# Optimization experiments

Measured on AMD Instinct MI355X. Metric: run time of the kernel, lower is better.

## Reference

```python
import jax, jax.numpy as jnp
import numpy as np

N = 6144
IN_F = 256
OUT_F = 64
ALPHA = 0.2  # leaky relu slope
NEG_INF = -9e15
ADJ_DENSITY = 0.01


def setup_inputs() -> dict:
    key = jax.random.key(0)
    kx, ka, kw, kat, ks, ke = jax.random.split(key, 6)
    x = jax.random.normal(kx, (N, IN_F), dtype=jnp.float32)
    adj = (jax.random.uniform(ka, (N, N)) < ADJ_DENSITY).astype(jnp.float32)
    adj = adj.at[jnp.arange(N), jnp.arange(N)].set(0.0)
    # xavier-uniform-ish init scale (gain 1.414)
    def xavier(k, shape):
        fan_in, fan_out = shape[0], shape[1]
        lim = 1.414 * np.sqrt(6.0 / (fan_in + fan_out))
        return jax.random.uniform(k, shape, minval=-lim, maxval=lim, dtype=jnp.float32)
    W = xavier(kw, (IN_F, OUT_F))
    a = xavier(kat, (2 * OUT_F, 1))
    W_si = xavier(ks, (1, 1))
    W_ei = xavier(ke, (1, 1))
    return {"x": x, "adj": adj, "W": W, "a": a, "W_si": W_si, "W_ei": W_ei}


def reference(x, adj, W, a, W_si, W_ei):
    # h: [N, F_out]
    h = x @ W
    # additive GAT score: e[i,j] = leakyrelu(Wh1[i] + Wh2[j])
    Wh1 = h @ a[:OUT_F, :]           # [N, 1]
    Wh2 = h @ a[OUT_F:, :]           # [N, 1]
    e = jax.nn.leaky_relu(Wh1 + Wh2.T, negative_slope=ALPHA)  # [N, N]
    # adjacency-power topology bias
    adj2 = adj @ adj
    adj3 = adj2 @ adj
    adj_w = adj + adj2 + adj3
    adj_w = adj_w.at[jnp.arange(N), jnp.arange(N)].set(0.0)
    e = jnp.abs(W_ei) * e + jnp.abs(W_si) * adj_w
    # masked softmax over neighbors (row-wise)
    scores = jnp.where(adj > 0, e, NEG_INF)
    attention = jax.nn.softmax(scores, axis=1)
    # dropout omitted (eval mode / training=False)
    h_prime = attention @ h
    return jax.nn.elu(h_prime)
```

## Files before the change

kernel.cpp:

```cpp
#include <hip/hip_runtime.h>
#include <math.h>

#define N 6144
#define MAXD 128
#define NWORDS 96
#define NW32 192

typedef unsigned long long u64;
typedef unsigned int u32;
typedef unsigned char u8;
typedef float f4 __attribute__((ext_vector_type(4)));


__device__ __forceinline__ int a_addr(int j) {
    int vdx = (j & ~255) | ((j & 3) << 6) | ((j >> 2) & 63);
    return (((vdx >> 2) & 7) << 10) | ((vdx >> 5) << 2) | (vdx & 3);
}

#define FA(s, c, a, b, ci) { u32 _t = (a) ^ (b); (s) = _t ^ (ci); (c) = ((a) & (b)) | ((ci) & _t); }

template <int START>
__device__ __forceinline__ void badd_from(u32* p, u32 cy) {
    #pragma unroll
    for (int q = START; q < 6; ++q) { u32 x = p[q] & cy; p[q] ^= cy; cy = x; }
    p[6] ^= cy;
}

__device__ __forceinline__ void csa15(u32* p, const u32* x) {
    u32 s0,c0,s1,c1,s2,c2,s3,c3,s4,c4;
    FA(s0,c0, x[0], x[1], x[2]);
    FA(s1,c1, x[3], x[4], x[5]);
    FA(s2,c2, x[6], x[7], x[8]);
    FA(s3,c3, x[9], x[10], x[11]);
    FA(s4,c4, x[12], x[13], x[14]);
    u32 t0,d0,u0,d1;
    FA(t0,d0, s0, s1, s2);
    FA(u0,d1, s3, s4, t0);
    u32 e0,f0,e1,f1,e2,f2;
    FA(e0,f0, c0, c1, c2);
    FA(e1,f1, c3, c4, d0);
    FA(e2,f2, e0, e1, d1);
    u32 g0,h0;
    FA(g0,h0, f0, f1, f2);
    badd_from<0>(p, u0);
    badd_from<1>(p, e2);
    badd_from<2>(p, g0);
    badd_from<3>(p, h0);
}

__device__ __forceinline__ u64 bit_transpose64(u64 x, int lane) {
    const u64 masks[6] = {0xAAAAAAAAAAAAAAAAull, 0xCCCCCCCCCCCCCCCCull,
                          0xF0F0F0F0F0F0F0F0ull, 0xFF00FF00FF00FF00ull,
                          0xFFFF0000FFFF0000ull, 0xFFFFFFFF00000000ull};
    #pragma unroll
    for (int k = 0; k < 6; ++k) {
        int s = 1 << k;
        u64 m = masks[k];
        u64 y = (u64)__shfl_xor((long long)x, s, 64);
        x = (lane & s) ? ((x & m) | ((y & m) >> s))
                       : ((x & ~m) | ((y & ~m) << s));
    }
    return x;
}

__global__ __launch_bounds__(256) void k_build(
    const float* __restrict__ adj,
    u64* __restrict__ rowbits, int* __restrict__ row_cnt, int* __restrict__ row_list)
{
    int i = blockIdx.x;
    int t = threadIdx.x, w = t >> 6, lane = t & 63;
    __shared__ int wtot[4];

    const f4* ar = (const f4*)(adj + (long)i * N) + (w * 6) * 64;

    f4 v[6];
    #pragma unroll
    for (int c = 0; c < 6; ++c)
        v[c] = __builtin_nontemporal_load(ar + c * 64 + lane);

    u64 m[6][4];
    #pragma unroll
    for (int c = 0; c < 6; ++c) {
        m[c][0] = __ballot(v[c].x != 0.0f);
        m[c][1] = __ballot(v[c].y != 0.0f);
        m[c][2] = __ballot(v[c].z != 0.0f);
        m[c][3] = __ballot(v[c].w != 0.0f);
    }

    int tot = 0;
    #pragma unroll
    for (int c = 0; c < 6; ++c) {
        #pragma unroll
        for (int p = 0; p < 4; ++p) tot += __popcll(m[c][p]);
    }
    if (lane == 0) wtot[w] = tot;
    __syncthreads();
    int base = 0;
    #pragma unroll
    for (int q = 0; q < 4; ++q) if (q < w) base += wtot[q];

    u64* rb = rowbits + (long)i * NWORDS + w * 24;
    #pragma unroll
    for (int c = 0; c < 6; ++c) {
        #pragma unroll
        for (int p = 0; p < 4; ++p) {
            u64 mm = m[c][p];
            if (lane == 0) rb[c * 4 + p] = mm;
            if ((mm >> lane) & 1ull) {
                int rank = __popcll(mm & ((1ull << lane) - 1ull));
                int s = base + rank;
                int j = (w * 6 + c) * 256 + (lane << 2) + p;
                if (s < MAXD) row_list[(long)i * MAXD + s] = j;
            }
            base += __popcll(mm);
        }
    }
    if (t == 0) {
        int tt = wtot[0] + wtot[1] + wtot[2] + wtot[3];
        row_cnt[i] = tt < 127 ? tt : 127;
    }
}

__global__ __launch_bounds__(256) void k_trans_gemm(
    const u64* __restrict__ rowbits, u64* __restrict__ colbits,
    const float* __restrict__ x, const float* __restrict__ W,
    const float* __restrict__ a,
    float* __restrict__ h, float* __restrict__ Wh1, float* __restrict__ Wh2)
{
    __shared__ float Wl[128 * 64];
    __shared__ float xt[8][256];

    int t = threadIdx.x, w = t >> 6, lane = t & 63;
    int bid = blockIdx.x;

    if (bid < 2304) {
        int tile = bid * 4 + w;
        int tr = tile / 96, tc = tile - tr * 96;
        u64 v = rowbits[(long)(tr * 64 + lane) * NWORDS + tc];
        v = bit_transpose64(v, lane);
        colbits[(long)(tc * 64 + lane) * NWORDS + tr] = v;
        return;
    }

    long i0 = (long)(bid - 2304) * 8;

    {
        const float4* xs = (const float4*)(x + i0 * 256);
        float4* xd = (float4*)&xt[0][0];
        xd[t]       = xs[t];
        xd[256 + t] = xs[256 + t];
    }

    float acc0 = 0.f, acc1 = 0.f;
    int r0 = w * 2;

    #pragma unroll
    for (int half = 0; half < 2; ++half) {
        __syncthreads();
        {
            const float4* Ws = (const float4*)(W + half * 128 * 64);
            float4* Wd = (float4*)Wl;
            #pragma unroll
            for (int q = 0; q < 8; ++q) Wd[q * 256 + t] = Ws[q * 256 + t];
        }
        __syncthreads();
        const float* xr0 = &xt[r0][half * 128];
        const float* xr1 = &xt[r0 + 1][half * 128];
        #pragma unroll 8
        for (int kk = 0; kk < 128; ++kk) {
            float wv = Wl[kk * 64 + lane];
            acc0 = fmaf(xr0[kk], wv, acc0);
            acc1 = fmaf(xr1[kk], wv, acc1);
        }
    }

    h[(i0 + r0)     * 64 + lane] = acc0;
    h[(i0 + r0 + 1) * 64 + lane] = acc1;
    float a1 = a[lane], a2 = a[64 + lane];
    float s10 = acc0 * a1, s20 = acc0 * a2;
    float s11 = acc1 * a1, s21 = acc1 * a2;
    #pragma unroll
    for (int off = 32; off; off >>= 1) {
        s10 += __shfl_xor(s10, off, 64);
        s20 += __shfl_xor(s20, off, 64);
        s11 += __shfl_xor(s11, off, 64);
        s21 += __shfl_xor(s21, off, 64);
    }
    if (lane == 0) {
        Wh1[i0 + r0]     = s10;  Wh2[i0 + r0]     = s20;
        Wh1[i0 + r0 + 1] = s11;  Wh2[i0 + r0 + 1] = s21;
    }
}

__global__ __launch_bounds__(256) void k_collist(
    const u64* __restrict__ colbits,
    int* __restrict__ col_cnt, int* __restrict__ col_list)
{
    int w = threadIdx.x >> 6, lane = threadIdx.x & 63;
    int v = blockIdx.x * 4 + w;
    int j = (v & ~255) | ((v & 63) << 2) | ((v >> 6) & 3);

    u64 w0 = 0, w1 = 0;
    if (lane < 48) {
        const u64* p2 = colbits + (long)v * NWORDS + lane * 2;
        w0 = p2[0]; w1 = p2[1];
    }
    int pc = __popcll(w0) + __popcll(w1);
    int incl = pc;
    #pragma unroll
    for (int off = 1; off < 64; off <<= 1) {
        int y = __shfl_up(incl, off, 64);
        if (lane >= off) incl += y;
    }
    int excl = incl - pc;
    int total = __shfl(incl, 63, 64);
    if (lane == 0) col_cnt[j] = total;

    int* cl = col_list + (long)j * MAXD;
    int s = excl;
    int ibase = lane * 128;
    while (w0) {
        int b = __ffsll((long long)w0) - 1; w0 &= w0 - 1;
        if (s < MAXD) cl[s] = a_addr(ibase + b);
        ++s;
    }
    ibase += 64;
    while (w1) {
        int b = __ffsll((long long)w1) - 1; w1 &= w1 - 1;
        if (s < MAXD) cl[s] = a_addr(ibase + b);
        ++s;
    }
}

__global__ __launch_bounds__(256) void k_attn(
    const float* __restrict__ h, const float* __restrict__ Wh1, const float* __restrict__ Wh2,
    const u64* __restrict__ rowbits,
    const int* __restrict__ row_cnt, const int* __restrict__ row_list,
    const int* __restrict__ col_cnt, const int* __restrict__ col_list,
    const float* __restrict__ W_si, const float* __restrict__ W_ei,
    float* __restrict__ out)
{
    __shared__ u32 adj2p[8 * 256];
    __shared__ int nbr[MAXD];
    __shared__ int ccbuf[MAXD];
    __shared__ float lrbuf[MAXD];
    __shared__ float ebuf[MAXD];
    __shared__ float part[256];
    __shared__ float sh_max, sh_sum;

    int i = blockIdx.x;
    int t = threadIdx.x, w = t >> 6, lane = t & 63;
    int deg = row_cnt[i];
    deg = deg < 127 ? deg : 127;

    if (deg == 0) {
        float acc = 0.f;
        for (int r = w; r < N; r += 4) acc += h[(long)r * 64 + lane];
        part[t] = acc;
        __syncthreads();
        if (w == 0) {
            float s = part[lane] + part[64 + lane] + part[128 + lane] + part[192 + lane];
            s *= (1.0f / N);
            out[(long)i * 64 + lane] = s > 0.f ? s : expm1f(s);
        }
        return;
    }

    float aWei = fabsf(W_ei[0]);
    float aWsi = fabsf(W_si[0]);

    if (t < deg) {
        int j = row_list[(long)i * MAXD + t];
        nbr[t] = j;
        int cc = col_cnt[j];
        ccbuf[t] = cc < MAXD ? cc : MAXD;
        float z = Wh1[i] + Wh2[j];
        lrbuf[t] = aWei * (z > 0.f ? z : 0.2f * z);
    }

    if (t < NW32) {
        const u32* rb32 = (const u32*)rowbits;
        const int* rl = row_list + (long)i * MAXD;
        u32 p[7] = {0,0,0,0,0,0,0};

        int m = 0;
        for (; m + 15 <= deg; m += 15) {
            u32 x[15];
            #pragma unroll
            for (int q = 0; q < 15; ++q) {
                int j = rl[m + q];
                x[q] = rb32[(long)j * NW32 + t];
            }
            csa15(p, x);
        }
        if (m < deg) {
            u32 x[15];
            #pragma unroll
            for (int q = 0; q < 15; ++q) {
                int mq = m + q;
                int j = rl[mq < deg ? mq : 0];
                u32 vv = rb32[(long)j * NW32 + t];
                x[q] = (mq < deg) ? vv : 0u;
            }
            csa15(p, x);
        }

        #pragma unroll
        for (int g = 0; g < 8; ++g) {
            u32 acc = 0;
            #pragma unroll
            for (int pl = 0; pl < 7; ++pl) {
                u32 nib = (p[pl] >> (4 * g)) & 0xFu;
                acc += (nib * (0x00204081u << pl)) & (0x01010101u << pl);
            }
            adj2p[g * 256 + t] = acc;
        }
    }
    __syncthreads();

    const u8* adj2b = (const u8*)adj2p;

    {
        int g = t >> 3, sub = t & 7;
        for (int e = g; e < deg; e += 32) {
            int cc = ccbuf[e];
            const int* cl = col_list + (long)nbr[e] * MAXD;
            u32 a30 = 0, a31 = 0, a32 = 0, a33 = 0;
            int q = sub;
            for (; q + 24 < cc; q += 32) {
                int k0 = cl[q];
                int k1 = cl[q + 8];
                int k2 = cl[q + 16];
                int k3 = cl[q + 24];
                a30 += (u32)adj2b[k0];
                a31 += (u32)adj2b[k1];
                a32 += (u32)adj2b[k2];
                a33 += (u32)adj2b[k3];
            }
            if (q + 8 < cc) {
                int k0 = cl[q];
                int k1 = cl[q + 8];
                a30 += (u32)adj2b[k0];
                a31 += (u32)adj2b[k1];
                q += 16;
            }
            if (q < cc) a32 += (u32)adj2b[cl[q]];
            u32 a3 = (a30 + a31) + (a32 + a33);
            a3 += __shfl_xor(a3, 1, 64);
            a3 += __shfl_xor(a3, 2, 64);
            a3 += __shfl_xor(a3, 4, 64);
            if (sub == 0) {
                u32 a2 = (u32)adj2b[a_addr(nbr[e])];
                ebuf[e] = lrbuf[e] + aWsi * (float)(1u + a2 + a3);
            }
        }
    }
    __syncthreads();

    if (w == 0) {
        float v = -3.4e38f;
        for (int idx = lane; idx < deg; idx += 64) v = fmaxf(v, ebuf[idx]);
        #pragma unroll
        for (int off = 32; off; off >>= 1) v = fmaxf(v, __shfl_xor(v, off, 64));
        if (lane == 0) sh_max = v;
    }
    __syncthreads();
    if (t < deg) ebuf[t] = expf(ebuf[t] - sh_max);
    __syncthreads();
    if (w == 0) {
        float s = 0.f;
        for (int idx = lane; idx < deg; idx += 64) s += ebuf[idx];
        #pragma unroll
        for (int off = 32; off; off >>= 1) s += __shfl_xor(s, off, 64);
        if (lane == 0) sh_sum = s;
    }
    __syncthreads();

    float acc0 = 0.f, acc1 = 0.f;
    int e = w;
    for (; e + 4 < deg; e += 8) {
        acc0 = fmaf(ebuf[e],     h[(long)nbr[e]     * 64 + lane], acc0);
        acc1 = fmaf(ebuf[e + 4], h[(long)nbr[e + 4] * 64 + lane], acc1);
    }
    if (e < deg)
        acc0 = fmaf(ebuf[e], h[(long)nbr[e] * 64 + lane], acc0);
    part[t] = acc0 + acc1;
    __syncthreads();
    if (w == 0) {
        float s = part[lane] + part[64 + lane] + part[128 + lane] + part[192 + lane];
        s /= sh_sum;
        out[(long)i * 64 + lane] = s > 0.f ? s : expm1f(s);
    }
}

extern "C" void kernel_launch(void* const* d_in, const int* in_sizes, int n_in,
                              void* d_out, int out_size, void* d_ws, size_t ws_size,
                              hipStream_t stream) {
    const float* x    = (const float*)d_in[0];
    const float* adj  = (const float*)d_in[1];
    const float* W    = (const float*)d_in[2];
    const float* a    = (const float*)d_in[3];
    const float* W_si = (const float*)d_in[4];
    const float* W_ei = (const float*)d_in[5];
    float* out = (float*)d_out;

    char* ws = (char*)d_ws;
    size_t off = 0;
    auto alloc = [&](size_t bytes) -> void* {
        void* p = ws + off;
        off += (bytes + 255) & ~(size_t)255;
        return p;
    };
    u64*   rowbits  = (u64*)  alloc((size_t)N * NWORDS * sizeof(u64));
    u64*   colbits  = (u64*)  alloc((size_t)N * NWORDS * sizeof(u64));
    float* h        = (float*)alloc((size_t)N * 64 * sizeof(float));
    float* Wh1      = (float*)alloc((size_t)N * sizeof(float));
    float* Wh2      = (float*)alloc((size_t)N * sizeof(float));
    int*   row_cnt  = (int*)  alloc((size_t)N * sizeof(int));
    int*   row_list = (int*)  alloc((size_t)N * MAXD * sizeof(int));
    int*   col_cnt  = (int*)  alloc((size_t)N * sizeof(int));
    int*   col_list = (int*)  alloc((size_t)N * MAXD * sizeof(int));

    k_build     <<<N, 256, 0, stream>>>(adj, rowbits, row_cnt, row_list);
    k_trans_gemm<<<2304 + 768, 256, 0, stream>>>(rowbits, colbits, x, W, a, h, Wh1, Wh2);
    k_collist   <<<N / 4, 256, 0, stream>>>(colbits, col_cnt, col_list);
    k_attn      <<<N, 256, 0, stream>>>(h, Wh1, Wh2, rowbits, row_cnt, row_list,
                                        col_cnt, col_list, W_si, W_ei, out);
}
```

Measured before the change: 294.0 us.

## Compute adj2 row via shared-memory atomic scatter instead of bitsliced CSA popcount

Replaces the bit-sliced carry-save adder that summed neighbor row bitmaps (reading 768 bytes per neighbor) with a sparse scatter. Each neighbor's row list is walked and a 6144-entry shared-memory counter is incremented with atomics. Column lists now store plain indices and the adj3 pass reads 32-bit counters. This trades dense bitmap loads and ALU work for about deg^2 LDS atomics and a 24KB shared buffer that must be zeroed per block, which may reduce occupancy.

```diff
diff --git a/kernel.cpp b/kernel.cpp
--- a/kernel.cpp
+++ b/kernel.cpp
@@ -4,49 +4,12 @@
 #define N 6144
 #define MAXD 128
 #define NWORDS 96
-#define NW32 192
 
 typedef unsigned long long u64;
 typedef unsigned int u32;
 typedef unsigned char u8;
 typedef float f4 __attribute__((ext_vector_type(4)));
 
-
-__device__ __forceinline__ int a_addr(int j) {
-    int vdx = (j & ~255) | ((j & 3) << 6) | ((j >> 2) & 63);
-    return (((vdx >> 2) & 7) << 10) | ((vdx >> 5) << 2) | (vdx & 3);
-}
-
-#define FA(s, c, a, b, ci) { u32 _t = (a) ^ (b); (s) = _t ^ (ci); (c) = ((a) & (b)) | ((ci) & _t); }
-
-template <int START>
-__device__ __forceinline__ void badd_from(u32* p, u32 cy) {
-    #pragma unroll
-    for (int q = START; q < 6; ++q) { u32 x = p[q] & cy; p[q] ^= cy; cy = x; }
-    p[6] ^= cy;
-}
-
-__device__ __forceinline__ void csa15(u32* p, const u32* x) {
-    u32 s0,c0,s1,c1,s2,c2,s3,c3,s4,c4;
-    FA(s0,c0, x[0], x[1], x[2]);
-    FA(s1,c1, x[3], x[4], x[5]);
-    FA(s2,c2, x[6], x[7], x[8]);
-    FA(s3,c3, x[9], x[10], x[11]);
-    FA(s4,c4, x[12], x[13], x[14]);
-    u32 t0,d0,u0,d1;
-    FA(t0,d0, s0, s1, s2);
-    FA(u0,d1, s3, s4, t0);
-    u32 e0,f0,e1,f1,e2,f2;
-    FA(e0,f0, c0, c1, c2);
-    FA(e1,f1, c3, c4, d0);
-    FA(e2,f2, e0, e1, d1);
-    u32 g0,h0;
-    FA(g0,h0, f0, f1, f2);
-    badd_from<0>(p, u0);
-    badd_from<1>(p, e2);
-    badd_from<2>(p, g0);
-    badd_from<3>(p, h0);
-}
 
 __device__ __forceinline__ u64 bit_transpose64(u64 x, int lane) {
     const u64 masks[6] = {0xAAAAAAAAAAAAAAAAull, 0xCCCCCCCCCCCCCCCCull,
@@ -221,28 +184,28 @@
     int ibase = lane * 128;
     while (w0) {
         int b = __ffsll((long long)w0) - 1; w0 &= w0 - 1;
-        if (s < MAXD) cl[s] = a_addr(ibase + b);
+        if (s < MAXD) cl[s] = ibase + b;
         ++s;
     }
     ibase += 64;
     while (w1) {
         int b = __ffsll((long long)w1) - 1; w1 &= w1 - 1;
-        if (s < MAXD) cl[s] = a_addr(ibase + b);
+        if (s < MAXD) cl[s] = ibase + b;
         ++s;
     }
 }
 
 __global__ __launch_bounds__(256) void k_attn(
     const float* __restrict__ h, const float* __restrict__ Wh1, const float* __restrict__ Wh2,
-    const u64* __restrict__ rowbits,
     const int* __restrict__ row_cnt, const int* __restrict__ row_list,
     const int* __restrict__ col_cnt, const int* __restrict__ col_list,
     const float* __restrict__ W_si, const float* __restrict__ W_ei,
     float* __restrict__ out)
 {
-    __shared__ u32 adj2p[8 * 256];
+    __shared__ __align__(16) u32 cnt[N];
     __shared__ int nbr[MAXD];
     __shared__ int ccbuf[MAXD];
+    __shared__ int rcbuf[MAXD];
     __shared__ float lrbuf[MAXD];
     __shared__ float ebuf[MAXD];
     __shared__ float part[256];
@@ -269,56 +232,34 @@
     float aWei = fabsf(W_ei[0]);
     float aWsi = fabsf(W_si[0]);
 
+    {
+        uint4 z = {0u, 0u, 0u, 0u};
+        uint4* c4 = (uint4*)cnt;
+        #pragma unroll
+        for (int q = 0; q < 6; ++q) c4[q * 256 + t] = z;
+    }
+
     if (t < deg) {
         int j = row_list[(long)i * MAXD + t];
         nbr[t] = j;
         int cc = col_cnt[j];
         ccbuf[t] = cc < MAXD ? cc : MAXD;
+        rcbuf[t] = row_cnt[j];
         float z = Wh1[i] + Wh2[j];
         lrbuf[t] = aWei * (z > 0.f ? z : 0.2f * z);
     }
-
-    if (t < NW32) {
-        const u32* rb32 = (const u32*)rowbits;
-        const int* rl = row_list + (long)i * MAXD;
-        u32 p[7] = {0,0,0,0,0,0,0};
-
-        int m = 0;
-        for (; m + 15 <= deg; m += 15) {
-            u32 x[15];
-            #pragma unroll
-            for (int q = 0; q < 15; ++q) {
-                int j = rl[m + q];
-                x[q] = rb32[(long)j * NW32 + t];
-            }
-            csa15(p, x);
-        }
-        if (m < deg) {
-            u32 x[15];
-            #pragma unroll
-            for (int q = 0; q < 15; ++q) {
-                int mq = m + q;
-                int j = rl[mq < deg ? mq : 0];
-                u32 vv = rb32[(long)j * NW32 + t];
-                x[q] = (mq < deg) ? vv : 0u;
-            }
-            csa15(p, x);
-        }
-
-        #pragma unroll
-        for (int g = 0; g < 8; ++g) {
-            u32 acc = 0;
-            #pragma unroll
-            for (int pl = 0; pl < 7; ++pl) {
-                u32 nib = (p[pl] >> (4 * g)) & 0xFu;
-                acc += (nib * (0x00204081u << pl)) & (0x01010101u << pl);
-            }
-            adj2p[g * 256 + t] = acc;
-        }
-    }
-    __syncthreads();
-
-    const u8* adj2b = (const u8*)adj2p;
+    __syncthreads();
+
+    {
+        int g = t >> 3, sub = t & 7;
+        for (int e = g; e < deg; e += 32) {
+            const int* rl = row_list + (long)nbr[e] * MAXD;
+            int rc = rcbuf[e];
+            for (int q = sub; q < rc; q += 8)
+                atomicAdd(&cnt[rl[q]], 1u);
+        }
+    }
+    __syncthreads();
 
     {
         int g = t >> 3, sub = t & 7;
@@ -332,25 +273,25 @@
                 int k1 = cl[q + 8];
                 int k2 = cl[q + 16];
                 int k3 = cl[q + 24];
-                a30 += (u32)adj2b[k0];
-                a31 += (u32)adj2b[k1];
-                a32 += (u32)adj2b[k2];
-                a33 += (u32)adj2b[k3];
+                a30 += cnt[k0];
+                a31 += cnt[k1];
+                a32 += cnt[k2];
+                a33 += cnt[k3];
             }
             if (q + 8 < cc) {
                 int k0 = cl[q];
                 int k1 = cl[q + 8];
-                a30 += (u32)adj2b[k0];
-                a31 += (u32)adj2b[k1];
+                a30 += cnt[k0];
+                a31 += cnt[k1];
                 q += 16;
             }
-            if (q < cc) a32 += (u32)adj2b[cl[q]];
+            if (q < cc) a32 += cnt[cl[q]];
             u32 a3 = (a30 + a31) + (a32 + a33);
             a3 += __shfl_xor(a3, 1, 64);
             a3 += __shfl_xor(a3, 2, 64);
             a3 += __shfl_xor(a3, 4, 64);
             if (sub == 0) {
-                u32 a2 = (u32)adj2b[a_addr(nbr[e])];
+                u32 a2 = cnt[nbr[e]];
                 ebuf[e] = lrbuf[e] + aWsi * (float)(1u + a2 + a3);
             }
         }
@@ -424,6 +365,6 @@
     k_build     <<<N, 256, 0, stream>>>(adj, rowbits, row_cnt, row_list);
     k_trans_gemm<<<2304 + 768, 256, 0, stream>>>(rowbits, colbits, x, W, a, h, Wh1, Wh2);
     k_collist   <<<N / 4, 256, 0, stream>>>(colbits, col_cnt, col_list);
-    k_attn      <<<N, 256, 0, stream>>>(h, Wh1, Wh2, rowbits, row_cnt, row_list,
+    k_attn      <<<N, 256, 0, stream>>>(h, Wh1, Wh2, row_cnt, row_list,
                                         col_cnt, col_list, W_si, W_ei, out);
 }
```

Result: slower. 319.7 us (+8.7%).

## Fuse bit transpose and column list build into GEMM kernel via shared memory

Applied to the files above, without the earlier changes.

The bit-matrix transpose now happens in shared memory, one block per 64-column stripe, and the column-list extraction runs in the same block instead of a separate kernel. This removes the global colbits buffer round trip and one kernel launch. In exchange only 96 blocks do the transpose and list work, each with a serial 24-iteration load loop and 16 list passes per wave, so parallelism there drops sharply. The shared-memory union also grows the GEMM blocks' footprint to about 50KB.

```diff
diff --git a/kernel.cpp b/kernel.cpp
--- a/kernel.cpp
+++ b/kernel.cpp
@@ -121,32 +121,74 @@
     }
 }
 
-__global__ __launch_bounds__(256) void k_trans_gemm(
-    const u64* __restrict__ rowbits, u64* __restrict__ colbits,
+__global__ __launch_bounds__(256) void k_csc_gemm(
+    const u64* __restrict__ rowbits,
+    int* __restrict__ col_cnt, int* __restrict__ col_list,
     const float* __restrict__ x, const float* __restrict__ W,
     const float* __restrict__ a,
     float* __restrict__ h, float* __restrict__ Wh1, float* __restrict__ Wh2)
 {
-    __shared__ float Wl[128 * 64];
-    __shared__ float xt[8][256];
+    __shared__ __align__(16) union SMem {
+        u64 colb[64][97];
+        struct { float Wl[128 * 64]; float xt[8][256]; } g;
+    } sm;
 
     int t = threadIdx.x, w = t >> 6, lane = t & 63;
     int bid = blockIdx.x;
 
-    if (bid < 2304) {
-        int tile = bid * 4 + w;
-        int tr = tile / 96, tc = tile - tr * 96;
-        u64 v = rowbits[(long)(tr * 64 + lane) * NWORDS + tc];
-        v = bit_transpose64(v, lane);
-        colbits[(long)(tc * 64 + lane) * NWORDS + tr] = v;
+    if (bid < 96) {
+        int c = bid;
+        for (int it = 0; it < 24; ++it) {
+            int tr = w * 24 + it;
+            u64 v = rowbits[(long)(tr * 64 + lane) * NWORDS + c];
+            v = bit_transpose64(v, lane);
+            sm.colb[lane][tr] = v;
+        }
+        __syncthreads();
+        for (int q0 = 0; q0 < 16; ++q0) {
+            int cidx = w * 16 + q0;
+            int v = c * 64 + cidx;
+            int j = (v & ~255) | ((v & 63) << 2) | ((v >> 6) & 3);
+
+            u64 w0 = 0, w1 = 0;
+            if (lane < 48) {
+                w0 = sm.colb[cidx][lane * 2];
+                w1 = sm.colb[cidx][lane * 2 + 1];
+            }
+            int pc = __popcll(w0) + __popcll(w1);
+            int incl = pc;
+            #pragma unroll
+            for (int off = 1; off < 64; off <<= 1) {
+                int y = __shfl_up(incl, off, 64);
+                if (lane >= off) incl += y;
+            }
+            int excl = incl - pc;
+            int total = __shfl(incl, 63, 64);
+            if (lane == 0) col_cnt[j] = total;
+
+            int* cl = col_list + (long)j * MAXD;
+            int s = excl;
+            int ibase = lane * 128;
+            while (w0) {
+                int b = __ffsll((long long)w0) - 1; w0 &= w0 - 1;
+                if (s < MAXD) cl[s] = a_addr(ibase + b);
+                ++s;
+            }
+            ibase += 64;
+            while (w1) {
+                int b = __ffsll((long long)w1) - 1; w1 &= w1 - 1;
+                if (s < MAXD) cl[s] = a_addr(ibase + b);
+                ++s;
+            }
+        }
         return;
     }
 
-    long i0 = (long)(bid - 2304) * 8;
+    long i0 = (long)(bid - 96) * 8;
 
     {
         const float4* xs = (const float4*)(x + i0 * 256);
-        float4* xd = (float4*)&xt[0][0];
+        float4* xd = (float4*)&sm.g.xt[0][0];
         xd[t]       = xs[t];
         xd[256 + t] = xs[256 + t];
     }
@@ -159,16 +201,16 @@
         __syncthreads();
         {
             const float4* Ws = (const float4*)(W + half * 128 * 64);
-            float4* Wd = (float4*)Wl;
+            float4* Wd = (float4*)sm.g.Wl;
             #pragma unroll
             for (int q = 0; q < 8; ++q) Wd[q * 256 + t] = Ws[q * 256 + t];
         }
         __syncthreads();
-        const float* xr0 = &xt[r0][half * 128];
-        const float* xr1 = &xt[r0 + 1][half * 128];
+        const float* xr0 = &sm.g.xt[r0][half * 128];
+        const float* xr1 = &sm.g.xt[r0 + 1][half * 128];
         #pragma unroll 8
         for (int kk = 0; kk < 128; ++kk) {
-            float wv = Wl[kk * 64 + lane];
+            float wv = sm.g.Wl[kk * 64 + lane];
             acc0 = fmaf(xr0[kk], wv, acc0);
             acc1 = fmaf(xr1[kk], wv, acc1);
         }
@@ -189,46 +231,6 @@
     if (lane == 0) {
         Wh1[i0 + r0]     = s10;  Wh2[i0 + r0]     = s20;
         Wh1[i0 + r0 + 1] = s11;  Wh2[i0 + r0 + 1] = s21;
-    }
-}
-
-__global__ __launch_bounds__(256) void k_collist(
-    const u64* __restrict__ colbits,
-    int* __restrict__ col_cnt, int* __restrict__ col_list)
-{
-    int w = threadIdx.x >> 6, lane = threadIdx.x & 63;
-    int v = blockIdx.x * 4 + w;
-    int j = (v & ~255) | ((v & 63) << 2) | ((v >> 6) & 3);
-
-    u64 w0 = 0, w1 = 0;
-    if (lane < 48) {
-        const u64* p2 = colbits + (long)v * NWORDS + lane * 2;
-        w0 = p2[0]; w1 = p2[1];
-    }
-    int pc = __popcll(w0) + __popcll(w1);
-    int incl = pc;
-    #pragma unroll
-    for (int off = 1; off < 64; off <<= 1) {
-        int y = __shfl_up(incl, off, 64);
-        if (lane >= off) incl += y;
-    }
-    int excl = incl - pc;
-    int total = __shfl(incl, 63, 64);
-    if (lane == 0) col_cnt[j] = total;
-
-    int* cl = col_list + (long)j * MAXD;
-    int s = excl;
-    int ibase = lane * 128;
-    while (w0) {
-        int b = __ffsll((long long)w0) - 1; w0 &= w0 - 1;
-        if (s < MAXD) cl[s] = a_addr(ibase + b);
-        ++s;
-    }
-    ibase += 64;
-    while (w1) {
-        int b = __ffsll((long long)w1) - 1; w1 &= w1 - 1;
-        if (s < MAXD) cl[s] = a_addr(ibase + b);
-        ++s;
     }
 }
 
@@ -412,7 +414,6 @@
         return p;
     };
     u64*   rowbits  = (u64*)  alloc((size_t)N * NWORDS * sizeof(u64));
-    u64*   colbits  = (u64*)  alloc((size_t)N * NWORDS * sizeof(u64));
     float* h        = (float*)alloc((size_t)N * 64 * sizeof(float));
     float* Wh1      = (float*)alloc((size_t)N * sizeof(float));
     float* Wh2      = (float*)alloc((size_t)N * sizeof(float));
@@ -421,9 +422,9 @@
     int*   col_cnt  = (int*)  alloc((size_t)N * sizeof(int));
     int*   col_list = (int*)  alloc((size_t)N * MAXD * sizeof(int));
 
-    k_build     <<<N, 256, 0, stream>>>(adj, rowbits, row_cnt, row_list);
-    k_trans_gemm<<<2304 + 768, 256, 0, stream>>>(rowbits, colbits, x, W, a, h, Wh1, Wh2);
-    k_collist   <<<N / 4, 256, 0, stream>>>(colbits, col_cnt, col_list);
-    k_attn      <<<N, 256, 0, stream>>>(h, Wh1, Wh2, rowbits, row_cnt, row_list,
-                                        col_cnt, col_list, W_si, W_ei, out);
-}
+    k_build   <<<N, 256, 0, stream>>>(adj, rowbits, row_cnt, row_list);
+    k_csc_gemm<<<96 + 768, 256, 0, stream>>>(rowbits, col_cnt, col_list,
+                                             x, W, a, h, Wh1, Wh2);
+    k_attn    <<<N, 256, 0, stream>>>(h, Wh1, Wh2, rowbits, row_cnt, row_list,
+                                      col_cnt, col_list, W_si, W_ei, out);
+}
```

New measurement: 304.8 us. 3.7% more time.

## Build column lists by atomic scatter from row lists instead of bit transpose

Applied to the files above, without the earlier changes.

Drops the 64x64 bit-matrix transpose into a colbits buffer and the separate column-list kernel. Column adjacency lists are now built directly from the row neighbor lists, using atomicAdd slot allocation on col_cnt. This work shares a launch with the x@W GEMM, and col_cnt is zeroed by a memset beforehand. It removes a multi-megabyte intermediate and one launch, but adds atomic contention and makes the order within each column list nondeterministic.

```diff
diff --git a/kernel.cpp b/kernel.cpp
--- a/kernel.cpp
+++ b/kernel.cpp
@@ -48,21 +48,6 @@
     badd_from<3>(p, h0);
 }
 
-__device__ __forceinline__ u64 bit_transpose64(u64 x, int lane) {
-    const u64 masks[6] = {0xAAAAAAAAAAAAAAAAull, 0xCCCCCCCCCCCCCCCCull,
-                          0xF0F0F0F0F0F0F0F0ull, 0xFF00FF00FF00FF00ull,
-                          0xFFFF0000FFFF0000ull, 0xFFFFFFFF00000000ull};
-    #pragma unroll
-    for (int k = 0; k < 6; ++k) {
-        int s = 1 << k;
-        u64 m = masks[k];
-        u64 y = (u64)__shfl_xor((long long)x, s, 64);
-        x = (lane & s) ? ((x & m) | ((y & m) >> s))
-                       : ((x & ~m) | ((y & ~m) << s));
-    }
-    return x;
-}
-
 __global__ __launch_bounds__(256) void k_build(
     const float* __restrict__ adj,
     u64* __restrict__ rowbits, int* __restrict__ row_cnt, int* __restrict__ row_list)
@@ -121,8 +106,9 @@
     }
 }
 
-__global__ __launch_bounds__(256) void k_trans_gemm(
-    const u64* __restrict__ rowbits, u64* __restrict__ colbits,
+__global__ __launch_bounds__(256) void k_csc_gemm(
+    const int* __restrict__ row_cnt, const int* __restrict__ row_list,
+    int* __restrict__ col_cnt, int* __restrict__ col_list,
     const float* __restrict__ x, const float* __restrict__ W,
     const float* __restrict__ a,
     float* __restrict__ h, float* __restrict__ Wh1, float* __restrict__ Wh2)
@@ -133,16 +119,21 @@
     int t = threadIdx.x, w = t >> 6, lane = t & 63;
     int bid = blockIdx.x;
 
-    if (bid < 2304) {
-        int tile = bid * 4 + w;
-        int tr = tile / 96, tc = tile - tr * 96;
-        u64 v = rowbits[(long)(tr * 64 + lane) * NWORDS + tc];
-        v = bit_transpose64(v, lane);
-        colbits[(long)(tc * 64 + lane) * NWORDS + tr] = v;
+    if (bid < 192) {
+        int i = bid * 32 + (t >> 3);
+        int sub = t & 7;
+        int deg = row_cnt[i];
+        int ai = a_addr(i);
+        const int* rl = row_list + (long)i * MAXD;
+        for (int e = sub; e < deg; e += 8) {
+            int j = rl[e];
+            int slot = atomicAdd(&col_cnt[j], 1);
+            if (slot < MAXD) col_list[(long)j * MAXD + slot] = ai;
+        }
         return;
     }
 
-    long i0 = (long)(bid - 2304) * 8;
+    long i0 = (long)(bid - 192) * 8;
 
     {
         const float4* xs = (const float4*)(x + i0 * 256);
@@ -189,46 +180,6 @@
     if (lane == 0) {
         Wh1[i0 + r0]     = s10;  Wh2[i0 + r0]     = s20;
         Wh1[i0 + r0 + 1] = s11;  Wh2[i0 + r0 + 1] = s21;
-    }
-}
-
-__global__ __launch_bounds__(256) void k_collist(
-    const u64* __restrict__ colbits,
-    int* __restrict__ col_cnt, int* __restrict__ col_list)
-{
-    int w = threadIdx.x >> 6, lane = threadIdx.x & 63;
-    int v = blockIdx.x * 4 + w;
-    int j = (v & ~255) | ((v & 63) << 2) | ((v >> 6) & 3);
-
-    u64 w0 = 0, w1 = 0;
-    if (lane < 48) {
-        const u64* p2 = colbits + (long)v * NWORDS + lane * 2;
-        w0 = p2[0]; w1 = p2[1];
-    }
-    int pc = __popcll(w0) + __popcll(w1);
-    int incl = pc;
-    #pragma unroll
-    for (int off = 1; off < 64; off <<= 1) {
-        int y = __shfl_up(incl, off, 64);
-        if (lane >= off) incl += y;
-    }
-    int excl = incl - pc;
-    int total = __shfl(incl, 63, 64);
-    if (lane == 0) col_cnt[j] = total;
-
-    int* cl = col_list + (long)j * MAXD;
-    int s = excl;
-    int ibase = lane * 128;
-    while (w0) {
-        int b = __ffsll((long long)w0) - 1; w0 &= w0 - 1;
-        if (s < MAXD) cl[s] = a_addr(ibase + b);
-        ++s;
-    }
-    ibase += 64;
-    while (w1) {
-        int b = __ffsll((long long)w1) - 1; w1 &= w1 - 1;
-        if (s < MAXD) cl[s] = a_addr(ibase + b);
-        ++s;
     }
 }
 
@@ -412,7 +363,6 @@
         return p;
     };
     u64*   rowbits  = (u64*)  alloc((size_t)N * NWORDS * sizeof(u64));
-    u64*   colbits  = (u64*)  alloc((size_t)N * NWORDS * sizeof(u64));
     float* h        = (float*)alloc((size_t)N * 64 * sizeof(float));
     float* Wh1      = (float*)alloc((size_t)N * sizeof(float));
     float* Wh2      = (float*)alloc((size_t)N * sizeof(float));
@@ -421,9 +371,11 @@
     int*   col_cnt  = (int*)  alloc((size_t)N * sizeof(int));
     int*   col_list = (int*)  alloc((size_t)N * MAXD * sizeof(int));
 
-    k_build     <<<N, 256, 0, stream>>>(adj, rowbits, row_cnt, row_list);
-    k_trans_gemm<<<2304 + 768, 256, 0, stream>>>(rowbits, colbits, x, W, a, h, Wh1, Wh2);
-    k_collist   <<<N / 4, 256, 0, stream>>>(colbits, col_cnt, col_list);
-    k_attn      <<<N, 256, 0, stream>>>(h, Wh1, Wh2, rowbits, row_cnt, row_list,
-                                        col_cnt, col_list, W_si, W_ei, out);
-}
+    hipMemsetAsync(col_cnt, 0, (size_t)N * sizeof(int), stream);
+
+    k_build   <<<N, 256, 0, stream>>>(adj, rowbits, row_cnt, row_list);
+    k_csc_gemm<<<192 + 768, 256, 0, stream>>>(row_cnt, row_list, col_cnt, col_list,
+                                              x, W, a, h, Wh1, Wh2);
+    k_attn    <<<N, 256, 0, stream>>>(h, Wh1, Wh2, rowbits, row_cnt, row_list,
+                                      col_cnt, col_list, W_si, W_ei, out);
+}
```

New measurement: 320.8 us. 1.09x slower.
